# Kernel tuning notes

Hardware: AMD Instinct MI355X
Metric: run time of the kernel (lower is better)

The kernel has to match this reference:

```python
import jax, jax.numpy as jnp
import numpy as np
import math

PI = math.pi
L = 6.0 * math.pi
EPS = 1e-5


def c19_activation(x, rho=4.0):
    scaled = x * (1.0 / PI)
    n = jnp.floor(scaled)
    t = scaled - n
    h = t * (1.0 - t)
    sgn = jnp.where(jnp.remainder(n, 2.0) < 1.0, 1.0, -1.0)
    core = PI * (sgn * h + rho * h * h)
    return jnp.where(x >= L, x - L, jnp.where(x <= -L, x + L, core))


def layer_norm(x, gamma, beta):
    mu = jnp.mean(x, axis=-1, keepdims=True)
    var = jnp.mean(jnp.square(x - mu), axis=-1, keepdims=True)
    return (x - mu) * jax.lax.rsqrt(var + EPS) * gamma + beta


def setup_inputs() -> dict:
    key = jax.random.key(0)
    ks = jax.random.split(key, 8)
    B, T, NB, D, DEPTH = 65536, 32, 8, 128, 4
    nl = DEPTH - 1  # 3 inner layers
    x = jax.random.normal(ks[0], (B, T, NB), dtype=jnp.float32)
    Wi = jax.random.normal(ks[1], (NB, D), dtype=jnp.float32) * 0.1   # input_proj (in, out)
    bi = jnp.zeros((D,), jnp.float32)
    Wo = jax.random.normal(ks[2], (D, NB), dtype=jnp.float32) * 0.1   # output_proj
    bo = jnp.zeros((NB,), jnp.float32)
    g_state = jnp.ones((D,), jnp.float32)
    b_state = jnp.zeros((D,), jnp.float32)
    Ws = jax.random.normal(ks[3], (nl, D, D), dtype=jnp.float32) * (1.0 / math.sqrt(D))
    bs = jnp.zeros((nl, D), jnp.float32)
    gs = jnp.ones((nl, D), jnp.float32)
    betas = jnp.zeros((nl, D), jnp.float32)
    return {"x": x, "Wi": Wi, "bi": bi, "Wo": Wo, "bo": bo,
            "g_state": g_state, "b_state": b_state,
            "Ws": Ws, "bs": bs, "gs": gs, "betas": betas}


def reference(x, Wi, bi, Wo, bo, g_state, b_state, Ws, bs, gs, betas):
    B, T, _ = x.shape
    D = Wi.shape[1]
    nl = Ws.shape[0]

    def step(h, xt):  # h: [B,D], xt: [B,NB]
        inp = xt @ Wi + bi
        state = 0.618 * layer_norm(h, g_state, b_state) + 0.382 * inp
        for i in range(nl):  # fixed small depth loop
            state = state + c19_activation(layer_norm(state, gs[i], betas[i]) @ Ws[i] + bs[i])
        out = state @ Wo + bo
        return state, out

    h0 = jnp.zeros((B, D), dtype=x.dtype)
    _, outs = jax.lax.scan(step, h0, jnp.swapaxes(x, 0, 1))  # outs: [T,B,NB]
    return jnp.swapaxes(outs, 0, 1)  # [B,T,NB]
```

## Files before the change

kernel.cpp:

```cpp
#include <hip/hip_runtime.h>
#include <math.h>

#define BDIM 1024
#define BR   64
#define D    128
#define SPD  130
#define WSP  130
#define SWOP 12
#define TT   32
#define NB   8
#define NL   3

typedef double v4d __attribute__((ext_vector_type(4)));

__device__ __forceinline__ double c19_act_d(double x) {
    const double PI_D = 3.14159265358979323846;
    const double L6   = 6.0 * PI_D;
    double scaled = x * (1.0 / PI_D);
    double n = floor(scaled);
    double t = scaled - n;
    double h = t * (1.0 - t);
    double halfn = n * 0.5;
    double fr = halfn - floor(halfn);
    double sgn = (fr < 0.25) ? 1.0 : -1.0;
    double core = PI_D * (sgn * h + 4.0 * h * h);
    double r = core;
    r = (x <= -L6) ? (x + L6) : r;
    r = (x >=  L6) ? (x - L6) : r;
    return r;
}

__global__ void miniphi_prep(const float* __restrict__ Ws, const float* __restrict__ gs,
                             double* __restrict__ wp) {
    int idx = blockIdx.x * 256 + threadIdx.x;
    wp[idx] = (double)gs[idx >> 7] * (double)Ws[idx];
}

__global__ __launch_bounds__(BDIM) void miniphi_kernel(
    const float* __restrict__ x,  const float* __restrict__ Wi, const float* __restrict__ bi,
    const float* __restrict__ Wo, const float* __restrict__ bo,
    const float* __restrict__ g_state, const float* __restrict__ b_state,
    const float* __restrict__ Ws, const float* __restrict__ bs,
    const float* __restrict__ gs, const float* __restrict__ betas,
    const double* __restrict__ wp,
    float* __restrict__ out)
{
    __shared__ double sState[BR][SPD];
    __shared__ double sWq[2][32][WSP];
    __shared__ float  sWi[NB][D];
    __shared__ float  sWo[D][SWOP];
    __shared__ float  sBi[D], sGst[D], sBst[D];
    __shared__ double sGsD[NL][D];
    __shared__ double sGW[NL][D];
    __shared__ double sBWbs[NL][D];
    __shared__ double sRstd[BR], sMu2[BR];
    __shared__ float  sBo[NB];
    __shared__ int    sPR[64][4], sPC[64][4];
    __shared__ int    sFlag;

    const int tid  = threadIdx.x;
    const int lane = tid & 63;
    const int wv   = tid >> 6;

    for (int i = tid; i < NB * D; i += BDIM) sWi[i >> 7][i & 127] = Wi[i];
    for (int i = tid; i < D * NB; i += BDIM) sWo[i >> 3][i & 7] = Wo[i];
    for (int i = tid; i < D; i += BDIM) { sBi[i] = bi[i]; sGst[i] = g_state[i]; sBst[i] = b_state[i]; }
    for (int i = tid; i < NL * D; i += BDIM) sGsD[i >> 7][i & 127] = (double)gs[i];
    if (tid < NB) sBo[tid] = bo[tid];
    for (int i = tid; i < BR * D; i += BDIM) sState[i >> 7][i & 127] = 0.0;
    if (tid < NL * D) {
        int ly = tid >> 7, c = tid & 127;
        const float* wl = Ws + (size_t)ly * D * D;
        double gw = 0.0, bw = 0.0;
        for (int k = 0; k < D; ++k) {
            double w = (double)wl[k * D + c];
            gw = fma((double)gs[ly * D + k], w, gw);
            bw = fma((double)betas[ly * D + k], w, bw);
        }
        sGW[ly][c] = gw;
        sBWbs[ly][c] = bw + (double)bs[ly * D + c];
    }

    if (wv == 0) {
        const int plm = lane & 15, plk = lane >> 4;
        v4d z = {0.0, 0.0, 0.0, 0.0};
        v4d p1 = __builtin_amdgcn_mfma_f64_16x16x4f64((double)plm, 1.0, z, 0, 0, 0);
        v4d p2 = __builtin_amdgcn_mfma_f64_16x16x4f64(1.0, (double)plm, z, 0, 0, 0);
        double pk = (double)(1 << plk);
        v4d p3 = __builtin_amdgcn_mfma_f64_16x16x4f64(pk, pk, z, 0, 0, 0);
        v4d p4 = __builtin_amdgcn_mfma_f64_16x16x4f64(1.0 + 0x1p-30, 1.0, z, 0, 0, 0);
        double pa5 = (plk == 0) ? 1.0 : 0x1p-52;
        v4d p5 = __builtin_amdgcn_mfma_f64_16x16x4f64(pa5, 1.0, z, 0, 0, 0);
        bool ok = true;
        #pragma unroll
        for (int i = 0; i < 4; ++i) {
            double v = p1[i]; int r = (int)(v * 0.25 + 0.5);
            ok = ok && (v == 4.0 * (double)r) && (r >= 0) && (r < 16);
            sPR[lane][i] = r;
            double w = p2[i]; int c2 = (int)(w * 0.25 + 0.5);
            ok = ok && (w == 4.0 * (double)c2) && (c2 >= 0) && (c2 < 16);
            sPC[lane][i] = c2;
            ok = ok && (p3[i] == 85.0);
            ok = ok && (p4[i] == 4.0 + 0x1p-28);
            ok = ok && (p5[i] == 1.0 + 3.0 * 0x1p-52);
        }
        unsigned long long bal = __ballot(ok ? 1 : 0);
        if (lane == 0) sFlag = (bal == 0xFFFFFFFFFFFFFFFFull) ? 1 : 0;
    }
    __syncthreads();
    const int useMfma = sFlag;

    const int rLN = tid >> 4;
    const int sL  = tid & 15;
    const int lm  = lane & 15, lk = lane >> 4;
    const int rb  = (wv >> 3) * 32;
    const int c0  = (wv & 7) * 16;
    const int r0v = wv * 4;
    const size_t rowg = (size_t)blockIdx.x * BR;

    #define STAGE_Q(LY, Q, QB)                                                      \
      { if (wp) {                                                                   \
          const double* src = wp + (((size_t)(LY) * D + (Q) * 32) * D);             \
          _Pragma("unroll")                                                         \
          for (int i_ = 0; i_ < 2; ++i_) {                                          \
              int kr_ = wv * 2 + i_;                                                \
              const double* g_ = src + (size_t)kr_ * D + lane * 2;                  \
              __builtin_amdgcn_global_load_lds(                                     \
                  (const __attribute__((address_space(1))) void*)g_,                \
                  (__attribute__((address_space(3))) void*)&sWq[QB][kr_][0],        \
                  16, 0, 0);                                                        \
          }                                                                         \
        } else {                                                                    \
          const float* src = Ws + (((size_t)(LY) * D + (Q) * 32) * D);              \
          const double* gl = &sGsD[LY][(Q) * 32];                                   \
          _Pragma("unroll")                                                         \
          for (int i_ = 0; i_ < 2; ++i_) {                                          \
              int kr_ = wv * 2 + i_;                                                \
              float2 w_ = *(const float2*)(src + (size_t)kr_ * D + lane * 2);       \
              double g_ = gl[kr_];                                                  \
              double2 o_; o_.x = g_ * (double)w_.x; o_.y = g_ * (double)w_.y;       \
              *(double2*)&sWq[QB][kr_][lane * 2] = o_;                              \
          }                                                                         \
        } }

    #define MFMA_Q(QB, QK)                                                          \
      { _Pragma("unroll")                                                           \
        for (int k0 = 0; k0 < 32; k0 += 4) {                                        \
            double b  = sWq[QB][k0 + lk][c0 + lm];                                  \
            double a0 = sState[rb + lm     ][(QK) + k0 + lk];                       \
            double a1 = sState[rb + lm + 16][(QK) + k0 + lk];                       \
            acc0 = __builtin_amdgcn_mfma_f64_16x16x4f64(a0, b, acc0, 0, 0, 0);      \
            acc1 = __builtin_amdgcn_mfma_f64_16x16x4f64(a1, b, acc1, 0, 0, 0);      \
        } }

    #define VALU_Q(QB, QK)                                                          \
      { _Pragma("unroll 4")                                                         \
        for (int kk = 0; kk < 32; kk += 2) {                                        \
            int kg = (QK) + kk;                                                     \
            double b00 = sWq[QB][kk][lane],     b01 = sWq[QB][kk][lane + 64];       \
            double b10 = sWq[QB][kk + 1][lane], b11 = sWq[QB][kk + 1][lane + 64];   \
            _Pragma("unroll")                                                       \
            for (int r = 0; r < 4; ++r) {                                           \
                double2 a = *(const double2*)&sState[r0v + r][kg];                  \
                accv[r][0] = fma(a.y, b10, fma(a.x, b00, accv[r][0]));              \
                accv[r][1] = fma(a.y, b11, fma(a.x, b01, accv[r][1]));              \
            }                                                                       \
        } }

    #define LN_BLOCK                                                                \
      { double sum = 0.0;                                                           \
        _Pragma("unroll")                                                           \
        for (int j = 0; j < 8; ++j) sum += sState[rLN][sL + 16 * j];                \
        sum += __shfl_xor(sum, 1); sum += __shfl_xor(sum, 2);                       \
        sum += __shfl_xor(sum, 4); sum += __shfl_xor(sum, 8);                       \
        double mu = sum * (1.0 / 128.0);                                            \
        double sq = 0.0;                                                            \
        _Pragma("unroll")                                                           \
        for (int j = 0; j < 8; ++j) { double dd = sState[rLN][sL + 16 * j] - mu; sq += dd * dd; } \
        sq += __shfl_xor(sq, 1); sq += __shfl_xor(sq, 2);                           \
        sq += __shfl_xor(sq, 4); sq += __shfl_xor(sq, 8);                           \
        double rstd = 1.0 / sqrt(sq * (1.0 / 128.0) + 1e-5);                        \
        if (sL == 0) { sRstd[rLN] = rstd; sMu2[rLN] = mu * rstd; } }

    STAGE_Q(0, 0, 0)

    for (int t = 0; t < TT; ++t) {
        {
            const float* xp = x + (rowg + (size_t)rLN) * (TT * NB) + (size_t)t * NB;
            float4 xa = *(const float4*)(xp);
            float4 xb = *(const float4*)(xp + 4);
            float xf[8] = {xa.x, xa.y, xa.z, xa.w, xb.x, xb.y, xb.z, xb.w};

            double sum = 0.0;
            #pragma unroll
            for (int j = 0; j < 8; ++j) sum += sState[rLN][sL + 16 * j];
            sum += __shfl_xor(sum, 1); sum += __shfl_xor(sum, 2);
            sum += __shfl_xor(sum, 4); sum += __shfl_xor(sum, 8);
            double mu = sum * (1.0 / 128.0);
            double sq = 0.0;
            #pragma unroll
            for (int j = 0; j < 8; ++j) { double dd = sState[rLN][sL + 16 * j] - mu; sq += dd * dd; }
            sq += __shfl_xor(sq, 1); sq += __shfl_xor(sq, 2);
            sq += __shfl_xor(sq, 4); sq += __shfl_xor(sq, 8);
            double rstd = 1.0 / sqrt(sq * (1.0 / 128.0) + 1e-5);

            #pragma unroll
            for (int j = 0; j < 8; ++j) {
                int c = sL + 16 * j;
                double v = sState[rLN][c];
                double inp = (double)sBi[c];
                #pragma unroll
                for (int k = 0; k < 8; ++k)
                    inp = fma((double)xf[k], (double)sWi[k][c], inp);
                double ln = (v - mu) * rstd * (double)sGst[c] + (double)sBst[c];
                sState[rLN][c] = 0.618 * ln + 0.382 * inp;
            }
        }
        __syncthreads();

        for (int ly = 0; ly < NL; ++ly) {
            if (useMfma) {
                v4d acc0 = {0,0,0,0}, acc1 = {0,0,0,0};
                STAGE_Q(ly, 1, 1)
                MFMA_Q(0, 0)
                LN_BLOCK
                __syncthreads();
                STAGE_Q(ly, 2, 0)  MFMA_Q(1, 32)  __syncthreads();
                STAGE_Q(ly, 3, 1)  MFMA_Q(0, 64)  __syncthreads();
                if (ly + 1 < NL) { STAGE_Q(ly + 1, 0, 0) } else { STAGE_Q(0, 0, 0) }
                MFMA_Q(1, 96)
                __syncthreads();
                #pragma unroll
                for (int i = 0; i < 4; ++i) {
                    int col = c0 + sPC[lane][i];
                    int R0  = rb + sPR[lane][i];
                    double gwc = sGW[ly][col], bwc = sBWbs[ly][col];
                    double y0 = fma(sRstd[R0],      acc0[i], fma(-sMu2[R0],      gwc, bwc));
                    double y1 = fma(sRstd[R0 + 16], acc1[i], fma(-sMu2[R0 + 16], gwc, bwc));
                    sState[R0][col]      += c19_act_d(y0);
                    sState[R0 + 16][col] += c19_act_d(y1);
                }
            } else {
                double accv[4][2];
                #pragma unroll
                for (int r = 0; r < 4; ++r) { accv[r][0] = 0.0; accv[r][1] = 0.0; }
                STAGE_Q(ly, 1, 1)
                VALU_Q(0, 0)
                LN_BLOCK
                __syncthreads();
                STAGE_Q(ly, 2, 0)  VALU_Q(1, 32)  __syncthreads();
                STAGE_Q(ly, 3, 1)  VALU_Q(0, 64)  __syncthreads();
                if (ly + 1 < NL) { STAGE_Q(ly + 1, 0, 0) } else { STAGE_Q(0, 0, 0) }
                VALU_Q(1, 96)
                __syncthreads();
                double gwc0 = sGW[ly][lane],   gwc1 = sGW[ly][lane + 64];
                double bwc0 = sBWbs[ly][lane], bwc1 = sBWbs[ly][lane + 64];
                #pragma unroll
                for (int r = 0; r < 4; ++r) {
                    int R = r0v + r;
                    double rs = sRstd[R], m2 = sMu2[R];
                    double y0 = fma(rs, accv[r][0], fma(-m2, gwc0, bwc0));
                    double y1 = fma(rs, accv[r][1], fma(-m2, gwc1, bwc1));
                    sState[R][lane]      += c19_act_d(y0);
                    sState[R][lane + 64] += c19_act_d(y1);
                }
            }
            __syncthreads();
        }

        #pragma unroll
        for (int p = 0; p < 2; ++p) {
            double accj[4] = {0.0, 0.0, 0.0, 0.0};
            #pragma unroll
            for (int u = 0; u < 8; ++u) {
                int k = sL + 16 * u;
                double s = sState[rLN][k];
                float4 w = *(const float4*)&sWo[k][4 * p];
                accj[0] = fma(s, (double)w.x, accj[0]);
                accj[1] = fma(s, (double)w.y, accj[1]);
                accj[2] = fma(s, (double)w.z, accj[2]);
                accj[3] = fma(s, (double)w.w, accj[3]);
            }
            #pragma unroll
            for (int j = 0; j < 4; ++j) {
                accj[j] += __shfl_xor(accj[j], 1);
                accj[j] += __shfl_xor(accj[j], 2);
                accj[j] += __shfl_xor(accj[j], 4);
                accj[j] += __shfl_xor(accj[j], 8);
            }
            int jloc = sL - 4 * p;
            double o = accj[0];
            #pragma unroll
            for (int j = 1; j < 4; ++j) o = (jloc == j) ? accj[j] : o;
            if (jloc >= 0 && jloc < 4)
                out[((rowg + (size_t)rLN) * TT + (size_t)t) * NB + sL] =
                    (float)(o + (double)sBo[sL]);
        }
    }
    #undef LN_BLOCK
    #undef VALU_Q
    #undef MFMA_Q
    #undef STAGE_Q
}

extern "C" void kernel_launch(void* const* d_in, const int* in_sizes, int n_in,
                              void* d_out, int out_size, void* d_ws, size_t ws_size,
                              hipStream_t stream) {
    const float* x       = (const float*)d_in[0];
    const float* Wi      = (const float*)d_in[1];
    const float* bi      = (const float*)d_in[2];
    const float* Wo      = (const float*)d_in[3];
    const float* bo      = (const float*)d_in[4];
    const float* g_state = (const float*)d_in[5];
    const float* b_state = (const float*)d_in[6];
    const float* Ws      = (const float*)d_in[7];
    const float* bs      = (const float*)d_in[8];
    const float* gs      = (const float*)d_in[9];
    const float* betas   = (const float*)d_in[10];
    float* out = (float*)d_out;

    const size_t wp_bytes = (size_t)NL * D * D * sizeof(double);
    double* wp = (ws_size >= wp_bytes) ? (double*)d_ws : nullptr;
    if (wp) {
        dim3 pgrid(NL * D * D / 256), pblock(256);
        hipLaunchKernelGGL(miniphi_prep, pgrid, pblock, 0, stream, Ws, gs, wp);
    }

    const int B = in_sizes[0] / (TT * NB);
    dim3 grid(B / BR), block(BDIM);
    hipLaunchKernelGGL(miniphi_kernel, grid, block, 0, stream,
                       x, Wi, bi, Wo, bo, g_state, b_state, Ws, bs, gs, betas, wp, out);
}
```

Before: 5.049 ms.

## Split matmul rows between MFMA and VALU wavefronts in hybrid scheme

Each block has 16 waves. Four of them (every fifth wave) now compute 16 rows of the 128x128 fp64 layer matmul with VALU FMAs. The other 12 waves use f64 MFMA on the remaining 48 rows, each producing a 16x32 tile instead of a 32x16 tile. The intent is to use the otherwise idle VALU pipes alongside the matrix cores and split the layer work across both. This makes wave roles and instruction counts uneven, and each layer phase is only as fast as the slower group.

```diff
diff --git a/kernel.cpp b/kernel.cpp
--- a/kernel.cpp
+++ b/kernel.cpp
@@ -113,9 +113,14 @@
     const int rLN = tid >> 4;
     const int sL  = tid & 15;
     const int lm  = lane & 15, lk = lane >> 4;
-    const int rb  = (wv >> 3) * 32;
-    const int c0  = (wv & 7) * 16;
-    const int r0v = wv * 4;
+    const int isValu = ((wv % 5) == 0);
+    const int hIdx   = wv / 5;
+    const int rH     = 48 + hIdx * 4;
+    const int m12    = wv - 1 - wv / 5;
+    const int rbm    = (m12 >> 2) * 16;
+    const int n0a    = (m12 & 3) * 32;
+    const int n0b    = n0a + 16;
+    const int r0v    = wv * 4;
     const size_t rowg = (size_t)blockIdx.x * BR;
 
     #define STAGE_Q(LY, Q, QB)                                                      \
@@ -143,14 +148,28 @@
           }                                                                         \
         } }
 
-    #define MFMA_Q(QB, QK)                                                          \
+    #define MFMA_H(QB, QK)                                                          \
       { _Pragma("unroll")                                                           \
         for (int k0 = 0; k0 < 32; k0 += 4) {                                        \
-            double b  = sWq[QB][k0 + lk][c0 + lm];                                  \
-            double a0 = sState[rb + lm     ][(QK) + k0 + lk];                       \
-            double a1 = sState[rb + lm + 16][(QK) + k0 + lk];                       \
-            acc0 = __builtin_amdgcn_mfma_f64_16x16x4f64(a0, b, acc0, 0, 0, 0);      \
-            acc1 = __builtin_amdgcn_mfma_f64_16x16x4f64(a1, b, acc1, 0, 0, 0);      \
+            double b0 = sWq[QB][k0 + lk][n0a + lm];                                 \
+            double b1 = sWq[QB][k0 + lk][n0b + lm];                                 \
+            double a  = sState[rbm + lm][(QK) + k0 + lk];                           \
+            acc0 = __builtin_amdgcn_mfma_f64_16x16x4f64(a, b0, acc0, 0, 0, 0);      \
+            acc1 = __builtin_amdgcn_mfma_f64_16x16x4f64(a, b1, acc1, 0, 0, 0);      \
+        } }
+
+    #define VALU_H(QB, QK)                                                          \
+      { _Pragma("unroll 4")                                                         \
+        for (int kk = 0; kk < 32; kk += 2) {                                        \
+            int kg = (QK) + kk;                                                     \
+            double b00 = sWq[QB][kk][lane],     b01 = sWq[QB][kk][lane + 64];       \
+            double b10 = sWq[QB][kk + 1][lane], b11 = sWq[QB][kk + 1][lane + 64];   \
+            _Pragma("unroll")                                                       \
+            for (int r = 0; r < 4; ++r) {                                           \
+                double2 a = *(const double2*)&sState[rH + r][kg];                   \
+                acc0[r] = fma(a.y, b10, fma(a.x, b00, acc0[r]));                    \
+                acc1[r] = fma(a.y, b11, fma(a.x, b01, acc1[r]));                    \
+            }                                                                       \
         } }
 
     #define VALU_Q(QB, QK)                                                          \
@@ -162,8 +181,8 @@
             _Pragma("unroll")                                                       \
             for (int r = 0; r < 4; ++r) {                                           \
                 double2 a = *(const double2*)&sState[r0v + r][kg];                  \
-                accv[r][0] = fma(a.y, b10, fma(a.x, b00, accv[r][0]));              \
-                accv[r][1] = fma(a.y, b11, fma(a.x, b01, accv[r][1]));              \
+                acc0[r] = fma(a.y, b10, fma(a.x, b00, acc0[r]));                    \
+                acc1[r] = fma(a.y, b11, fma(a.x, b01, acc1[r]));                    \
             }                                                                       \
         } }
 
@@ -222,28 +241,44 @@
             if (useMfma) {
                 v4d acc0 = {0,0,0,0}, acc1 = {0,0,0,0};
                 STAGE_Q(ly, 1, 1)
-                MFMA_Q(0, 0)
+                if (!isValu) { MFMA_H(0, 0) } else { VALU_H(0, 0) }
                 LN_BLOCK
                 __syncthreads();
-                STAGE_Q(ly, 2, 0)  MFMA_Q(1, 32)  __syncthreads();
-                STAGE_Q(ly, 3, 1)  MFMA_Q(0, 64)  __syncthreads();
+                STAGE_Q(ly, 2, 0)
+                if (!isValu) { MFMA_H(1, 32) } else { VALU_H(1, 32) }
+                __syncthreads();
+                STAGE_Q(ly, 3, 1)
+                if (!isValu) { MFMA_H(0, 64) } else { VALU_H(0, 64) }
+                __syncthreads();
                 if (ly + 1 < NL) { STAGE_Q(ly + 1, 0, 0) } else { STAGE_Q(0, 0, 0) }
-                MFMA_Q(1, 96)
-                __syncthreads();
-                #pragma unroll
-                for (int i = 0; i < 4; ++i) {
-                    int col = c0 + sPC[lane][i];
-                    int R0  = rb + sPR[lane][i];
-                    double gwc = sGW[ly][col], bwc = sBWbs[ly][col];
-                    double y0 = fma(sRstd[R0],      acc0[i], fma(-sMu2[R0],      gwc, bwc));
-                    double y1 = fma(sRstd[R0 + 16], acc1[i], fma(-sMu2[R0 + 16], gwc, bwc));
-                    sState[R0][col]      += c19_act_d(y0);
-                    sState[R0 + 16][col] += c19_act_d(y1);
+                if (!isValu) { MFMA_H(1, 96) } else { VALU_H(1, 96) }
+                __syncthreads();
+                if (!isValu) {
+                    #pragma unroll
+                    for (int i = 0; i < 4; ++i) {
+                        int col0 = n0a + sPC[lane][i];
+                        int col1 = n0b + sPC[lane][i];
+                        int R0   = rbm + sPR[lane][i];
+                        double rs = sRstd[R0], m2 = sMu2[R0];
+                        double y0 = fma(rs, acc0[i], fma(-m2, sGW[ly][col0], sBWbs[ly][col0]));
+                        double y1 = fma(rs, acc1[i], fma(-m2, sGW[ly][col1], sBWbs[ly][col1]));
+                        sState[R0][col0] += c19_act_d(y0);
+                        sState[R0][col1] += c19_act_d(y1);
+                    }
+                } else {
+                    #pragma unroll
+                    for (int r = 0; r < 4; ++r) {
+                        int R = rH + r;
+                        double rs = sRstd[R], m2 = sMu2[R];
+                        double y0 = fma(rs, acc0[r], fma(-m2, sGW[ly][lane],      sBWbs[ly][lane]));
+                        double y1 = fma(rs, acc1[r], fma(-m2, sGW[ly][lane + 64], sBWbs[ly][lane + 64]));
+                        sState[R][lane]      += c19_act_d(y0);
+                        sState[R][lane + 64] += c19_act_d(y1);
+                    }
                 }
+                __syncthreads();
             } else {
-                double accv[4][2];
-                #pragma unroll
-                for (int r = 0; r < 4; ++r) { accv[r][0] = 0.0; accv[r][1] = 0.0; }
+                v4d acc0 = {0,0,0,0}, acc1 = {0,0,0,0};
                 STAGE_Q(ly, 1, 1)
                 VALU_Q(0, 0)
                 LN_BLOCK
@@ -259,13 +294,13 @@
                 for (int r = 0; r < 4; ++r) {
                     int R = r0v + r;
                     double rs = sRstd[R], m2 = sMu2[R];
-                    double y0 = fma(rs, accv[r][0], fma(-m2, gwc0, bwc0));
-                    double y1 = fma(rs, accv[r][1], fma(-m2, gwc1, bwc1));
+                    double y0 = fma(rs, acc0[r], fma(-m2, gwc0, bwc0));
+                    double y1 = fma(rs, acc1[r], fma(-m2, gwc1, bwc1));
                     sState[R][lane]      += c19_act_d(y0);
                     sState[R][lane + 64] += c19_act_d(y1);
                 }
+                __syncthreads();
             }
-            __syncthreads();
         }
 
         #pragma unroll
@@ -299,7 +334,8 @@
     }
     #undef LN_BLOCK
     #undef VALU_Q
-    #undef MFMA_Q
+    #undef VALU_H
+    #undef MFMA_H
     #undef STAGE_Q
 }
 
```

Result: slower. 8.225 ms (+62.9%).

## Load MFMA weight operands directly from global/L2 instead of staging through LDS

Applied to the files above, without the earlier changes.

Removes the double-buffered LDS staging of the pre-scaled weight matrix (sWq) and the extra barriers between quarter-K chunks. Each wave now reads its B operands for the f64 MFMA straight from the precomputed global weight buffer, relying on L1/L2 caching since all blocks share the same small weights. This frees a large amount of shared memory, which may raise occupancy, and cuts syncthreads per layer. In exchange, every wave issues strided global loads per timestep, so latency is exposed unless it is hidden by the extra occupancy.

```diff
diff --git a/kernel.cpp b/kernel.cpp
--- a/kernel.cpp
+++ b/kernel.cpp
@@ -5,7 +5,6 @@
 #define BR   64
 #define D    128
 #define SPD  130
-#define WSP  130
 #define SWOP 12
 #define TT   32
 #define NB   8
@@ -46,11 +45,9 @@
     float* __restrict__ out)
 {
     __shared__ double sState[BR][SPD];
-    __shared__ double sWq[2][32][WSP];
     __shared__ float  sWi[NB][D];
     __shared__ float  sWo[D][SWOP];
     __shared__ float  sBi[D], sGst[D], sBst[D];
-    __shared__ double sGsD[NL][D];
     __shared__ double sGW[NL][D];
     __shared__ double sBWbs[NL][D];
     __shared__ double sRstd[BR], sMu2[BR];
@@ -65,7 +62,6 @@
     for (int i = tid; i < NB * D; i += BDIM) sWi[i >> 7][i & 127] = Wi[i];
     for (int i = tid; i < D * NB; i += BDIM) sWo[i >> 3][i & 7] = Wo[i];
     for (int i = tid; i < D; i += BDIM) { sBi[i] = bi[i]; sGst[i] = g_state[i]; sBst[i] = b_state[i]; }
-    for (int i = tid; i < NL * D; i += BDIM) sGsD[i >> 7][i & 127] = (double)gs[i];
     if (tid < NB) sBo[tid] = bo[tid];
     for (int i = tid; i < BR * D; i += BDIM) sState[i >> 7][i & 127] = 0.0;
     if (tid < NL * D) {
@@ -108,7 +104,7 @@
         if (lane == 0) sFlag = (bal == 0xFFFFFFFFFFFFFFFFull) ? 1 : 0;
     }
     __syncthreads();
-    const int useMfma = sFlag;
+    const int useMfma = sFlag && (wp != nullptr);
 
     const int rLN = tid >> 4;
     const int sL  = tid & 15;
@@ -117,55 +113,6 @@
     const int c0  = (wv & 7) * 16;
     const int r0v = wv * 4;
     const size_t rowg = (size_t)blockIdx.x * BR;
-
-    #define STAGE_Q(LY, Q, QB)                                                      \
-      { if (wp) {                                                                   \
-          const double* src = wp + (((size_t)(LY) * D + (Q) * 32) * D);             \
-          _Pragma("unroll")                                                         \
-          for (int i_ = 0; i_ < 2; ++i_) {                                          \
-              int kr_ = wv * 2 + i_;                                                \
-              const double* g_ = src + (size_t)kr_ * D + lane * 2;                  \
-              __builtin_amdgcn_global_load_lds(                                     \
-                  (const __attribute__((address_space(1))) void*)g_,                \
-                  (__attribute__((address_space(3))) void*)&sWq[QB][kr_][0],        \
-                  16, 0, 0);                                                        \
-          }                                                                         \
-        } else {                                                                    \
-          const float* src = Ws + (((size_t)(LY) * D + (Q) * 32) * D);              \
-          const double* gl = &sGsD[LY][(Q) * 32];                                   \
-          _Pragma("unroll")                                                         \
-          for (int i_ = 0; i_ < 2; ++i_) {                                          \
-              int kr_ = wv * 2 + i_;                                                \
-              float2 w_ = *(const float2*)(src + (size_t)kr_ * D + lane * 2);       \
-              double g_ = gl[kr_];                                                  \
-              double2 o_; o_.x = g_ * (double)w_.x; o_.y = g_ * (double)w_.y;       \
-              *(double2*)&sWq[QB][kr_][lane * 2] = o_;                              \
-          }                                                                         \
-        } }
-
-    #define MFMA_Q(QB, QK)                                                          \
-      { _Pragma("unroll")                                                           \
-        for (int k0 = 0; k0 < 32; k0 += 4) {                                        \
-            double b  = sWq[QB][k0 + lk][c0 + lm];                                  \
-            double a0 = sState[rb + lm     ][(QK) + k0 + lk];                       \
-            double a1 = sState[rb + lm + 16][(QK) + k0 + lk];                       \
-            acc0 = __builtin_amdgcn_mfma_f64_16x16x4f64(a0, b, acc0, 0, 0, 0);      \
-            acc1 = __builtin_amdgcn_mfma_f64_16x16x4f64(a1, b, acc1, 0, 0, 0);      \
-        } }
-
-    #define VALU_Q(QB, QK)                                                          \
-      { _Pragma("unroll 4")                                                         \
-        for (int kk = 0; kk < 32; kk += 2) {                                        \
-            int kg = (QK) + kk;                                                     \
-            double b00 = sWq[QB][kk][lane],     b01 = sWq[QB][kk][lane + 64];       \
-            double b10 = sWq[QB][kk + 1][lane], b11 = sWq[QB][kk + 1][lane + 64];   \
-            _Pragma("unroll")                                                       \
-            for (int r = 0; r < 4; ++r) {                                           \
-                double2 a = *(const double2*)&sState[r0v + r][kg];                  \
-                accv[r][0] = fma(a.y, b10, fma(a.x, b00, accv[r][0]));              \
-                accv[r][1] = fma(a.y, b11, fma(a.x, b01, accv[r][1]));              \
-            }                                                                       \
-        } }
 
     #define LN_BLOCK                                                                \
       { double sum = 0.0;                                                           \
@@ -182,7 +129,18 @@
         double rstd = 1.0 / sqrt(sq * (1.0 / 128.0) + 1e-5);                        \
         if (sL == 0) { sRstd[rLN] = rstd; sMu2[rLN] = mu * rstd; } }
 
-    STAGE_Q(0, 0, 0)
+    #define MFMA_QR(QK)                                                             \
+      { double b_[8];                                                               \
+        _Pragma("unroll")                                                           \
+        for (int i_ = 0; i_ < 8; ++i_)                                              \
+            b_[i_] = bsrc[(size_t)((QK) + i_ * 4 + lk) * D];                        \
+        _Pragma("unroll")                                                           \
+        for (int i_ = 0; i_ < 8; ++i_) {                                            \
+            double a0 = sState[rb + lm     ][(QK) + i_ * 4 + lk];                   \
+            double a1 = sState[rb + lm + 16][(QK) + i_ * 4 + lk];                   \
+            acc0 = __builtin_amdgcn_mfma_f64_16x16x4f64(a0, b_[i_], acc0, 0, 0, 0); \
+            acc1 = __builtin_amdgcn_mfma_f64_16x16x4f64(a1, b_[i_], acc1, 0, 0, 0); \
+        } }
 
     for (int t = 0; t < TT; ++t) {
         {
@@ -221,14 +179,12 @@
         for (int ly = 0; ly < NL; ++ly) {
             if (useMfma) {
                 v4d acc0 = {0,0,0,0}, acc1 = {0,0,0,0};
-                STAGE_Q(ly, 1, 1)
-                MFMA_Q(0, 0)
+                const double* bsrc = wp + (size_t)ly * D * D + c0 + lm;
+                MFMA_QR(0)
+                MFMA_QR(32)
+                MFMA_QR(64)
+                MFMA_QR(96)
                 LN_BLOCK
-                __syncthreads();
-                STAGE_Q(ly, 2, 0)  MFMA_Q(1, 32)  __syncthreads();
-                STAGE_Q(ly, 3, 1)  MFMA_Q(0, 64)  __syncthreads();
-                if (ly + 1 < NL) { STAGE_Q(ly + 1, 0, 0) } else { STAGE_Q(0, 0, 0) }
-                MFMA_Q(1, 96)
                 __syncthreads();
                 #pragma unroll
                 for (int i = 0; i < 4; ++i) {
@@ -241,17 +197,31 @@
                     sState[R0 + 16][col] += c19_act_d(y1);
                 }
             } else {
-                double accv[4][2];
-                #pragma unroll
-                for (int r = 0; r < 4; ++r) { accv[r][0] = 0.0; accv[r][1] = 0.0; }
-                STAGE_Q(ly, 1, 1)
-                VALU_Q(0, 0)
+                double acc0[4] = {0,0,0,0}, acc1[4] = {0,0,0,0};
+                const size_t lyb = (size_t)ly * D * D;
+                #pragma unroll 4
+                for (int kg = 0; kg < D; kg += 2) {
+                    double b00, b01, b10, b11;
+                    if (wp) {
+                        b00 = wp[lyb + (size_t)kg * D + lane];
+                        b01 = wp[lyb + (size_t)kg * D + lane + 64];
+                        b10 = wp[lyb + (size_t)(kg + 1) * D + lane];
+                        b11 = wp[lyb + (size_t)(kg + 1) * D + lane + 64];
+                    } else {
+                        double g0 = (double)gs[ly * D + kg], g1 = (double)gs[ly * D + kg + 1];
+                        b00 = g0 * (double)Ws[lyb + (size_t)kg * D + lane];
+                        b01 = g0 * (double)Ws[lyb + (size_t)kg * D + lane + 64];
+                        b10 = g1 * (double)Ws[lyb + (size_t)(kg + 1) * D + lane];
+                        b11 = g1 * (double)Ws[lyb + (size_t)(kg + 1) * D + lane + 64];
+                    }
+                    #pragma unroll
+                    for (int r = 0; r < 4; ++r) {
+                        double2 a = *(const double2*)&sState[r0v + r][kg];
+                        acc0[r] = fma(a.y, b10, fma(a.x, b00, acc0[r]));
+                        acc1[r] = fma(a.y, b11, fma(a.x, b01, acc1[r]));
+                    }
+                }
                 LN_BLOCK
-                __syncthreads();
-                STAGE_Q(ly, 2, 0)  VALU_Q(1, 32)  __syncthreads();
-                STAGE_Q(ly, 3, 1)  VALU_Q(0, 64)  __syncthreads();
-                if (ly + 1 < NL) { STAGE_Q(ly + 1, 0, 0) } else { STAGE_Q(0, 0, 0) }
-                VALU_Q(1, 96)
                 __syncthreads();
                 double gwc0 = sGW[ly][lane],   gwc1 = sGW[ly][lane + 64];
                 double bwc0 = sBWbs[ly][lane], bwc1 = sBWbs[ly][lane + 64];
@@ -259,8 +229,8 @@
                 for (int r = 0; r < 4; ++r) {
                     int R = r0v + r;
                     double rs = sRstd[R], m2 = sMu2[R];
-                    double y0 = fma(rs, accv[r][0], fma(-m2, gwc0, bwc0));
-                    double y1 = fma(rs, accv[r][1], fma(-m2, gwc1, bwc1));
+                    double y0 = fma(rs, acc0[r], fma(-m2, gwc0, bwc0));
+                    double y1 = fma(rs, acc1[r], fma(-m2, gwc1, bwc1));
                     sState[R][lane]      += c19_act_d(y0);
                     sState[R][lane + 64] += c19_act_d(y1);
                 }
@@ -297,10 +267,8 @@
                     (float)(o + (double)sBo[sL]);
         }
     }
+    #undef MFMA_QR
     #undef LN_BLOCK
-    #undef VALU_Q
-    #undef MFMA_Q
-    #undef STAGE_Q
 }
 
 extern "C" void kernel_launch(void* const* d_in, const int* in_sizes, int n_in,
```

New measurement: 5.065 ms. Within noise of the previous version (+0.3%).
